# Kernel tuning notes

Hardware: AMD Instinct MI355X
Metric: run time of the kernel (lower is better)

The kernel has to match this reference:

```python
import jax, jax.numpy as jnp
import numpy as np

B, NA, NL, D = 512, 128, 512, 128
KA, KL = 16, 16  # active_agents, lane_tokens


def _layernorm(x, g, b, eps=1e-5):
    m = x.mean(-1, keepdims=True)
    v = ((x - m) ** 2).mean(-1, keepdims=True)
    return (x - m) / jnp.sqrt(v + eps) * g + b


def setup_inputs() -> dict:
    key = jax.random.key(0)
    ks = jax.random.split(key, 16)
    s = D ** -0.5
    inp = {
        "actor_feat": jax.random.normal(ks[0], (B, NA, D), jnp.float32),
        "lane_feat": jax.random.normal(ks[1], (B, NL, D), jnp.float32),
        "lane_centers": jax.random.normal(ks[2], (B, NL, 2), jnp.float32) * 50.0,
        "x_centers": jax.random.normal(ks[3], (B, NA, 2), jnp.float32) * 50.0,
        "spike_rate": jax.random.uniform(ks[4], (B, NA), jnp.float32),
        "actor_valid": jax.random.randint(ks[5], (B, NA), 0, 2).astype(bool),
        "lane_valid": jax.random.randint(ks[6], (B, NL), 0, 2).astype(bool),
        # MLP layer 0
        "W0a": jax.random.normal(ks[7], (D, D), jnp.float32) * s,
        "b0a": jnp.zeros((D,), jnp.float32),
        "W0b": jax.random.normal(ks[8], (D, D), jnp.float32) * s,
        "b0b": jnp.zeros((D,), jnp.float32),
        # MLP layer 1
        "W1a": jax.random.normal(ks[9], (D, D), jnp.float32) * s,
        "b1a": jnp.zeros((D,), jnp.float32),
        "W1b": jax.random.normal(ks[10], (D, D), jnp.float32) * s,
        "b1b": jnp.zeros((D,), jnp.float32),
        # shared LayerNorm
        "gamma": jnp.ones((D,), jnp.float32),
        "beta": jnp.zeros((D,), jnp.float32),
    }
    return inp


def reference(actor_feat, lane_feat, lane_centers, x_centers, spike_rate,
              actor_valid, lane_valid,
              W0a, b0a, W0b, b0b, W1a, b1a, W1b, b1b, gamma, beta):
    bsel = jnp.arange(B)[:, None]  # [B,1] batch index for fancy gather/scatter

    # masked top-k over spike_rate -> active agent indices [B,KA]
    masked = jnp.where(actor_valid, spike_rate, -jnp.inf)
    _, aidx = jax.lax.top_k(masked, KA)

    # lane selection: min distance from any active agent, k smallest
    ac = x_centers[bsel, aidx]                                # [B,KA,2]
    diff = ac[:, :, None, :] - lane_centers[:, None, :, :]    # [B,KA,NL,2]
    pair_dist = jnp.sqrt((diff ** 2).sum(-1))                 # cdist [B,KA,NL]
    lane_dist = pair_dist.min(axis=1)                         # [B,NL]
    lane_dist = jnp.where(lane_valid, lane_dist, jnp.inf)
    _, lidx = jax.lax.top_k(-lane_dist, KL)                   # k smallest

    # gather nodes and run residual MLP + LayerNorm stack
    nodes = jnp.concatenate([actor_feat[bsel, aidx], lane_feat[bsel, lidx]], axis=1)  # [B,KA+KL,D]
    for (Wa, ba, Wb, bb) in ((W0a, b0a, W0b, b0b), (W1a, b1a, W1b, b1b)):
        h = jax.nn.gelu(nodes @ Wa + ba, approximate=False) @ Wb + bb
        nodes = _layernorm(nodes + h, gamma, beta)

    # scatter updated nodes back into the full pools
    actor_out = actor_feat.at[bsel, aidx].set(nodes[:, :KA])
    lane_out = lane_feat.at[bsel, lidx].set(nodes[:, KA:])
    return actor_out, lane_out
```

## Files before the change

kernel.cpp:

```cpp
#include <hip/hip_runtime.h>
#include <math.h>

#define Bsz 512
#define NA  128
#define NL  512
#define Dd  128
#define KA  16
#define KL  16

#define NMLP  256
#define NCOPY 1280
#define PAIRS (Bsz * 320)

#define AIDX_OFF  0
#define LIDX_OFF  8192
#define AMASK_OFF 16384
#define LMASK_OFF 18432
#define FLAG_OFF  26624

typedef float nf4 __attribute__((ext_vector_type(4)));

__global__ __launch_bounds__(256) void detect_bool_kernel(
    const unsigned char* __restrict__ av, int* __restrict__ flag) {
  __shared__ int s;
  if (threadIdx.x == 0) s = 0;
  __syncthreads();
  int any = 0;
  for (int i = threadIdx.x; i < 4096; i += 256)
    if ((i & 3) && av[i]) any = 1;
  if (any) atomicOr(&s, 1);
  __syncthreads();
  if (threadIdx.x == 0) *flag = s;
}

__device__ __forceinline__ int validAt(const unsigned char* p, int i, int isbyte) {
  return isbyte ? (int)p[i] : ((const int*)p)[i];
}

__global__ __launch_bounds__(256) void idx_kernel(
    const float* __restrict__ spike, const unsigned char* __restrict__ avalid,
    const float* __restrict__ xc, const float* __restrict__ lc,
    const unsigned char* __restrict__ lvalid, const int* __restrict__ flagp,
    int* __restrict__ aidx, int* __restrict__ lidx,
    unsigned* __restrict__ amask_g, unsigned* __restrict__ lmask_g) {
  const int b = blockIdx.x;
  const int tid = threadIdx.x;
  const int isbyte = *flagp;

  __shared__ float s_ax[KA], s_ay[KA];
  __shared__ int   s_ai[KA];
  __shared__ int   s_li[KL];
  __shared__ float s_ld[NL];
  __shared__ float s_rv[4];
  __shared__ int   s_ri[4];
  __shared__ unsigned s_am[4], s_lm[16];

  if (tid < 64) {
    float v0 = validAt(avalid, b * NA + tid, isbyte)      ? spike[b * NA + tid]      : -INFINITY;
    float v1 = validAt(avalid, b * NA + tid + 64, isbyte) ? spike[b * NA + tid + 64] : -INFINITY;
    for (int it = 0; it < KA; ++it) {
      float bv = v0; int bi = tid;
      if (v1 > bv) { bv = v1; bi = tid + 64; }
      for (int off = 32; off; off >>= 1) {
        float ov = __shfl_xor(bv, off);
        int   oi = __shfl_xor(bi, off);
        if (ov > bv || (ov == bv && oi < bi)) { bv = ov; bi = oi; }
      }
      if (bi == tid)      v0 = -INFINITY;
      if (bi == tid + 64) v1 = -INFINITY;
      if (tid == 0) s_ai[it] = bi;
    }
  }
  __syncthreads();
  if (tid < KA) {
    int a = s_ai[tid];
    aidx[b * KA + tid] = a;
    s_ax[tid] = xc[(b * NA + a) * 2 + 0];
    s_ay[tid] = xc[(b * NA + a) * 2 + 1];
  }
  __syncthreads();

  for (int l = tid; l < NL; l += 256) {
    float lx = lc[(b * NL + l) * 2 + 0];
    float ly = lc[(b * NL + l) * 2 + 1];
    float best = INFINITY;
#pragma unroll
    for (int a = 0; a < KA; ++a) {
      float dx = s_ax[a] - lx, dy = s_ay[a] - ly;
      float d2 = __fadd_rn(__fmul_rn(dx, dx), __fmul_rn(dy, dy));
      best = fminf(best, d2);
    }
    best = sqrtf(best);
    s_ld[l] = validAt(lvalid, b * NL + l, isbyte) ? best : INFINITY;
  }
  __syncthreads();

  const int wid = tid >> 6, lane = tid & 63;
  for (int it = 0; it < KL; ++it) {
    float bv = s_ld[tid]; int bi = tid;
    float v2 = s_ld[tid + 256];
    if (v2 < bv) { bv = v2; bi = tid + 256; }
    for (int off = 32; off; off >>= 1) {
      float ov = __shfl_xor(bv, off);
      int   oi = __shfl_xor(bi, off);
      if (ov < bv || (ov == bv && oi < bi)) { bv = ov; bi = oi; }
    }
    if (lane == 0) { s_rv[wid] = bv; s_ri[wid] = bi; }
    __syncthreads();
    if (tid == 0) {
      float fbv = s_rv[0]; int fbi = s_ri[0];
      for (int w = 1; w < 4; ++w)
        if (s_rv[w] < fbv || (s_rv[w] == fbv && s_ri[w] < fbi)) { fbv = s_rv[w]; fbi = s_ri[w]; }
      lidx[b * KL + it] = fbi;
      s_li[it] = fbi;
      s_ld[fbi] = INFINITY;
    }
    __syncthreads();
  }

  if (tid < 4)  s_am[tid] = 0u;
  if (tid < 16) s_lm[tid] = 0u;
  __syncthreads();
  if (tid < 16) {
    int a = s_ai[tid];
    atomicOr(&s_am[a >> 5], 1u << (a & 31));
  } else if (tid < 32) {
    int l = s_li[tid - 16];
    atomicOr(&s_lm[l >> 5], 1u << (l & 31));
  }
  __syncthreads();
  if (tid < 4)  amask_g[b * 4 + tid]  = s_am[tid];
  if (tid < 16) lmask_g[b * 16 + tid] = s_lm[tid];
}


#define STAGE_LOAD(W, h)                                              \
  { const float4* wg4 = (const float4*)((W) + (h) * 8192);            \
    R0 = wg4[tid]; R1 = wg4[512 + tid];                               \
    R2 = wg4[1024 + tid]; R3 = wg4[1536 + tid]; }

#define STAGE_WRITE()                                                 \
  { float4* swg4 = (float4*)s_w;                                      \
    swg4[tid] = R0; swg4[512 + tid] = R1;                             \
    swg4[1024 + tid] = R2; swg4[1536 + tid] = R3; }

#define FMA_HALF(h)                                                   \
  _Pragma("unroll 4")                                                 \
  for (int g = 0; g < 16; ++g) {                                      \
    const float* wr = s_w + g * 4 * Dd;                               \
    float w00 = wr[j0],        w10 = wr[j1];                          \
    float w01 = wr[Dd + j0],   w11 = wr[Dd + j1];                     \
    float w02 = wr[2*Dd + j0], w12 = wr[2*Dd + j1];                   \
    float w03 = wr[3*Dd + j0], w13 = wr[3*Dd + j1];                   \
    _Pragma("unroll")                                                 \
    for (int n = 0; n < 8; ++n) {                                     \
      float4 xv = ((const float4*)s_xu[n0 + n])[(h) * 16 + g];        \
      acc0[n] = fmaf(xv.x, w00, acc0[n]); acc1[n] = fmaf(xv.x, w10, acc1[n]); \
      acc0[n] = fmaf(xv.y, w01, acc0[n]); acc1[n] = fmaf(xv.y, w11, acc1[n]); \
      acc0[n] = fmaf(xv.z, w02, acc0[n]); acc1[n] = fmaf(xv.z, w12, acc1[n]); \
      acc0[n] = fmaf(xv.w, w03, acc0[n]); acc1[n] = fmaf(xv.w, w13, acc1[n]); \
    }                                                                 \
  }

#define MATVEC(W, Bv)                                                 \
  { const float bias0 = (Bv)[j0], bias1 = (Bv)[j1];                   \
    _Pragma("unroll")                                                 \
    for (int n = 0; n < 8; ++n) { acc0[n] = bias0; acc1[n] = bias1; } \
    STAGE_LOAD(W, 0);                                                 \
    STAGE_WRITE(); __syncthreads();                                   \
    STAGE_LOAD(W, 1);                                                 \
    FMA_HALF(0);                                                      \
    __syncthreads();                                                  \
    STAGE_WRITE(); __syncthreads();                                   \
    FMA_HALF(1);                                                      \
    __syncthreads(); }

__global__ __launch_bounds__(512, 4) void fused_kernel(
    const float* __restrict__ actor_feat, const float* __restrict__ lane_feat,
    const int* __restrict__ aidx, const int* __restrict__ lidx,
    const unsigned* __restrict__ amask_g, const unsigned* __restrict__ lmask_g,
    const float* __restrict__ W0a, const float* __restrict__ b0a,
    const float* __restrict__ W0b, const float* __restrict__ b0b,
    const float* __restrict__ W1a, const float* __restrict__ b1a,
    const float* __restrict__ W1b, const float* __restrict__ b1b,
    const float* __restrict__ gamma, const float* __restrict__ beta,
    float* __restrict__ out0, float* __restrict__ out1) {
  __shared__ float s_w[64 * Dd];
  __shared__ float s_xu[64][Dd];
  __shared__ int   s_src[64];

  const int tid = threadIdx.x;
  const int wave = tid >> 6, lane = tid & 63;

  if (blockIdx.x < NMLP) {
    const int b0 = blockIdx.x * 2;
    if (tid < 64) {
      int rr = tid, bidx = b0 + (rr >> 5), lr = rr & 31;
      s_src[rr] = (lr < 16) ? aidx[bidx * KA + lr] : lidx[bidx * KL + lr - 16];
    }
    __syncthreads();

    const int n0 = wave * 8;
#pragma unroll
    for (int i = 0; i < 4; ++i) {
      int q = lane + 64 * i;
      int rr = n0 + (q >> 5), c4 = q & 31;
      int bidx = b0 + (rr >> 5), lr = rr & 31;
      const float* src = (lr < 16)
          ? actor_feat + ((size_t)bidx * NA + s_src[rr]) * Dd
          : lane_feat  + ((size_t)bidx * NL + s_src[rr]) * Dd;
      ((float4*)s_xu[rr])[c4] = ((const float4*)src)[c4];
    }

    const int j0 = lane, j1 = lane + 64;
    const float g0 = gamma[j0], g1 = gamma[j1];
    const float bt0 = beta[j0], bt1 = beta[j1];

    float acc0[8], acc1[8], rx0[8], rx1[8];
    float4 R0, R1, R2, R3;

#pragma unroll
    for (int n = 0; n < 8; ++n) {
      rx0[n] = s_xu[n0 + n][j0];
      rx1[n] = s_xu[n0 + n][j1];
    }

#pragma unroll 1
    for (int layer = 0; layer < 2; ++layer) {
      const float* wa = layer ? W1a : W0a;
      const float* ba = layer ? b1a : b0a;
      const float* wb = layer ? W1b : W0b;
      const float* bb = layer ? b1b : b0b;

      MATVEC(wa, ba);

#pragma unroll
      for (int n = 0; n < 8; ++n) {
        float t0 = acc0[n], t1 = acc1[n];
        s_xu[n0 + n][j0] = 0.5f * t0 * (1.0f + erff(t0 * 0.70710678118654752f));
        s_xu[n0 + n][j1] = 0.5f * t1 * (1.0f + erff(t1 * 0.70710678118654752f));
      }

      MATVEC(wb, bb);

#pragma unroll
      for (int n = 0; n < 8; ++n) {
        float r0 = rx0[n] + acc0[n];
        float r1 = rx1[n] + acc1[n];
        float sum = r0 + r1;
        for (int off = 32; off; off >>= 1) sum += __shfl_xor(sum, off);
        float mean = sum * (1.0f / 128.0f);
        float d0 = r0 - mean, d1 = r1 - mean;
        float sq = d0 * d0 + d1 * d1;
        for (int off = 32; off; off >>= 1) sq += __shfl_xor(sq, off);
        float inv = 1.0f / sqrtf(sq * (1.0f / 128.0f) + 1e-5f);
        float v0 = d0 * inv * g0 + bt0;
        float v1 = d1 * inv * g1 + bt1;
        if (layer == 0) {
          s_xu[n0 + n][j0] = v0; s_xu[n0 + n][j1] = v1;
          rx0[n] = v0; rx1[n] = v1;
        } else {
          int rr = n0 + n, bidx = b0 + (rr >> 5), lr = rr & 31, si = s_src[rr];
          float* dst = (lr < 16) ? out0 + ((size_t)bidx * NA + si) * Dd
                                 : out1 + ((size_t)bidx * NL + si) * Dd;
          dst[j0] = v0;
          dst[j1] = v1;
        }
      }
    }
  } else {
    const int gw = (blockIdx.x - NMLP) * 8 + wave;
    const int half = lane >> 5, c4 = lane & 31;
#pragma unroll 1
    for (int base = gw * 4; base < PAIRS; base += NCOPY * 8 * 4) {
      nf4 v[4]; int sel[4];
      const nf4* sp[4]; nf4* dp[4];
#pragma unroll
      for (int u = 0; u < 4; ++u) {
        int p = base + u;
        sel[u] = 1; sp[u] = 0; dp[u] = 0;
        if (p < PAIRS) {
          int b = p / 320;
          int pr = p - b * 320;
          int r = 2 * pr + half;
          unsigned mword; size_t prow;
          const float* srcpool; float* dstpool; int rbit;
          if (r < NA) {
            rbit = r;
            mword = amask_g[b * 4 + (r >> 5)];
            prow = (size_t)b * NA + r;
            srcpool = actor_feat; dstpool = out0;
          } else {
            int rl = r - NA;
            rbit = rl;
            mword = lmask_g[b * 16 + (rl >> 5)];
            prow = (size_t)b * NL + rl;
            srcpool = lane_feat; dstpool = out1;
          }
          sel[u] = (mword >> (rbit & 31)) & 1;
          sp[u] = (const nf4*)(srcpool + prow * Dd) + c4;
          dp[u] = (nf4*)(dstpool + prow * Dd) + c4;
          if (!sel[u]) v[u] = __builtin_nontemporal_load(sp[u]);
        }
      }
#pragma unroll
      for (int u = 0; u < 4; ++u)
        if (!sel[u]) __builtin_nontemporal_store(v[u], dp[u]);
    }
  }
}

extern "C" void kernel_launch(void* const* d_in, const int* in_sizes, int n_in,
                              void* d_out, int out_size, void* d_ws, size_t ws_size,
                              hipStream_t stream) {
  const float* actor_feat = (const float*)d_in[0];
  const float* lane_feat  = (const float*)d_in[1];
  const float* lc         = (const float*)d_in[2];
  const float* xc         = (const float*)d_in[3];
  const float* spike      = (const float*)d_in[4];
  const unsigned char* avalid = (const unsigned char*)d_in[5];
  const unsigned char* lvalid = (const unsigned char*)d_in[6];
  const float* W0a = (const float*)d_in[7];
  const float* b0a = (const float*)d_in[8];
  const float* W0b = (const float*)d_in[9];
  const float* b0b = (const float*)d_in[10];
  const float* W1a = (const float*)d_in[11];
  const float* b1a = (const float*)d_in[12];
  const float* W1b = (const float*)d_in[13];
  const float* b1b = (const float*)d_in[14];
  const float* gamma = (const float*)d_in[15];
  const float* beta  = (const float*)d_in[16];

  int* wsI = (int*)d_ws;
  int* aidx = wsI + AIDX_OFF;
  int* lidx = wsI + LIDX_OFF;
  unsigned* amask_g = (unsigned*)(wsI + AMASK_OFF);
  unsigned* lmask_g = (unsigned*)(wsI + LMASK_OFF);
  int* flag = wsI + FLAG_OFF;

  float* out0 = (float*)d_out;
  float* out1 = out0 + (size_t)Bsz * NA * Dd;

  detect_bool_kernel<<<1, 256, 0, stream>>>(avalid, flag);
  idx_kernel<<<Bsz, 256, 0, stream>>>(spike, avalid, xc, lc, lvalid, flag,
                                      aidx, lidx, amask_g, lmask_g);
  fused_kernel<<<NMLP + NCOPY, 512, 0, stream>>>(
      actor_feat, lane_feat, aidx, lidx, amask_g, lmask_g,
      W0a, b0a, W0b, b0b, W1a, b1a, W1b, b1b, gamma, beta, out0, out1);
}
```

Measured before the change: 122.3 us.

## Overlap full-pool copy with index selection and drop mask-based selective copy

```diff
diff --git a/kernel.cpp b/kernel.cpp
--- a/kernel.cpp
+++ b/kernel.cpp
@@ -8,56 +8,72 @@
 #define KA  16
 #define KL  16
 
-#define NMLP  256
-#define NCOPY 1280
-#define PAIRS (Bsz * 320)
-
-#define AIDX_OFF  0
-#define LIDX_OFF  8192
-#define AMASK_OFF 16384
-#define LMASK_OFF 18432
-#define FLAG_OFF  26624
-
-typedef float nf4 __attribute__((ext_vector_type(4)));
-
-__global__ __launch_bounds__(256) void detect_bool_kernel(
-    const unsigned char* __restrict__ av, int* __restrict__ flag) {
-  __shared__ int s;
-  if (threadIdx.x == 0) s = 0;
-  __syncthreads();
-  int any = 0;
-  for (int i = threadIdx.x; i < 4096; i += 256)
-    if ((i & 3) && av[i]) any = 1;
-  if (any) atomicOr(&s, 1);
-  __syncthreads();
-  if (threadIdx.x == 0) *flag = s;
-}
-
-__device__ __forceinline__ int validAt(const unsigned char* p, int i, int isbyte) {
-  return isbyte ? (int)p[i] : ((const int*)p)[i];
-}
-
-__global__ __launch_bounds__(256) void idx_kernel(
+#define NIDX  512
+#define NCB   3584
+#define ACT4  2097152
+#define TOT4  10485760
+#define CSTRIDE (NCB * 256)
+
+__global__ __launch_bounds__(256) void idx_copy_kernel(
     const float* __restrict__ spike, const unsigned char* __restrict__ avalid,
     const float* __restrict__ xc, const float* __restrict__ lc,
-    const unsigned char* __restrict__ lvalid, const int* __restrict__ flagp,
+    const unsigned char* __restrict__ lvalid,
+    const float* __restrict__ actor_feat, const float* __restrict__ lane_feat,
     int* __restrict__ aidx, int* __restrict__ lidx,
-    unsigned* __restrict__ amask_g, unsigned* __restrict__ lmask_g) {
+    float* __restrict__ out0, float* __restrict__ out1) {
+  const int tid = threadIdx.x;
+
+  if (blockIdx.x >= NIDX) {
+    const float4* __restrict__ srcA = (const float4*)actor_feat;
+    const float4* __restrict__ srcL = (const float4*)lane_feat;
+    float4* __restrict__ dstA = (float4*)out0;
+    float4* __restrict__ dstL = (float4*)out1;
+    const int gid = (blockIdx.x - NIDX) * 256 + tid;
+#pragma unroll 1
+    for (int base = gid; base < TOT4; base += 4 * CSTRIDE) {
+      float4 v[4]; int pp[4];
+#pragma unroll
+      for (int u = 0; u < 4; ++u) {
+        pp[u] = base + u * CSTRIDE;
+        if (pp[u] < TOT4)
+          v[u] = (pp[u] < ACT4) ? srcA[pp[u]] : srcL[pp[u] - ACT4];
+      }
+#pragma unroll
+      for (int u = 0; u < 4; ++u) {
+        if (pp[u] < TOT4) {
+          if (pp[u] < ACT4) dstA[pp[u]] = v[u];
+          else              dstL[pp[u] - ACT4] = v[u];
+        }
+      }
+    }
+    return;
+  }
+
   const int b = blockIdx.x;
-  const int tid = threadIdx.x;
-  const int isbyte = *flagp;
 
   __shared__ float s_ax[KA], s_ay[KA];
   __shared__ int   s_ai[KA];
-  __shared__ int   s_li[KL];
   __shared__ float s_ld[NL];
   __shared__ float s_rv[4];
   __shared__ int   s_ri[4];
-  __shared__ unsigned s_am[4], s_lm[16];
+  __shared__ int   s_flag;
+
+  if (tid == 0) s_flag = 0;
+  __syncthreads();
+  {
+    int any = 0;
+    for (int i = tid; i < 4096; i += 256)
+      if ((i & 3) && avalid[i]) any = 1;
+    if (any) atomicOr(&s_flag, 1);
+  }
+  __syncthreads();
+  const int isbyte = s_flag;
+
+#define VALID_AT(P, I) (isbyte ? (int)(P)[I] : ((const int*)(P))[I])
 
   if (tid < 64) {
-    float v0 = validAt(avalid, b * NA + tid, isbyte)      ? spike[b * NA + tid]      : -INFINITY;
-    float v1 = validAt(avalid, b * NA + tid + 64, isbyte) ? spike[b * NA + tid + 64] : -INFINITY;
+    float v0 = VALID_AT(avalid, b * NA + tid)      ? spike[b * NA + tid]      : -INFINITY;
+    float v1 = VALID_AT(avalid, b * NA + tid + 64) ? spike[b * NA + tid + 64] : -INFINITY;
     for (int it = 0; it < KA; ++it) {
       float bv = v0; int bi = tid;
       if (v1 > bv) { bv = v1; bi = tid + 64; }
@@ -91,7 +107,7 @@
       best = fminf(best, d2);
     }
     best = sqrtf(best);
-    s_ld[l] = validAt(lvalid, b * NL + l, isbyte) ? best : INFINITY;
+    s_ld[l] = VALID_AT(lvalid, b * NL + l) ? best : INFINITY;
   }
   __syncthreads();
 
@@ -112,25 +128,11 @@
       for (int w = 1; w < 4; ++w)
         if (s_rv[w] < fbv || (s_rv[w] == fbv && s_ri[w] < fbi)) { fbv = s_rv[w]; fbi = s_ri[w]; }
       lidx[b * KL + it] = fbi;
-      s_li[it] = fbi;
       s_ld[fbi] = INFINITY;
     }
     __syncthreads();
   }
-
-  if (tid < 4)  s_am[tid] = 0u;
-  if (tid < 16) s_lm[tid] = 0u;
-  __syncthreads();
-  if (tid < 16) {
-    int a = s_ai[tid];
-    atomicOr(&s_am[a >> 5], 1u << (a & 31));
-  } else if (tid < 32) {
-    int l = s_li[tid - 16];
-    atomicOr(&s_lm[l >> 5], 1u << (l & 31));
-  }
-  __syncthreads();
-  if (tid < 4)  amask_g[b * 4 + tid]  = s_am[tid];
-  if (tid < 16) lmask_g[b * 16 + tid] = s_lm[tid];
+#undef VALID_AT
 }
 
 
@@ -175,10 +177,9 @@
     FMA_HALF(1);                                                      \
     __syncthreads(); }
 
-__global__ __launch_bounds__(512, 4) void fused_kernel(
+__global__ __launch_bounds__(512, 2) void mlp_kernel(
     const float* __restrict__ actor_feat, const float* __restrict__ lane_feat,
     const int* __restrict__ aidx, const int* __restrict__ lidx,
-    const unsigned* __restrict__ amask_g, const unsigned* __restrict__ lmask_g,
     const float* __restrict__ W0a, const float* __restrict__ b0a,
     const float* __restrict__ W0b, const float* __restrict__ b0b,
     const float* __restrict__ W1a, const float* __restrict__ b1a,
@@ -191,121 +192,80 @@
 
   const int tid = threadIdx.x;
   const int wave = tid >> 6, lane = tid & 63;
-
-  if (blockIdx.x < NMLP) {
-    const int b0 = blockIdx.x * 2;
-    if (tid < 64) {
-      int rr = tid, bidx = b0 + (rr >> 5), lr = rr & 31;
-      s_src[rr] = (lr < 16) ? aidx[bidx * KA + lr] : lidx[bidx * KL + lr - 16];
-    }
-    __syncthreads();
-
-    const int n0 = wave * 8;
-#pragma unroll
-    for (int i = 0; i < 4; ++i) {
-      int q = lane + 64 * i;
-      int rr = n0 + (q >> 5), c4 = q & 31;
-      int bidx = b0 + (rr >> 5), lr = rr & 31;
-      const float* src = (lr < 16)
-          ? actor_feat + ((size_t)bidx * NA + s_src[rr]) * Dd
-          : lane_feat  + ((size_t)bidx * NL + s_src[rr]) * Dd;
-      ((float4*)s_xu[rr])[c4] = ((const float4*)src)[c4];
-    }
-
-    const int j0 = lane, j1 = lane + 64;
-    const float g0 = gamma[j0], g1 = gamma[j1];
-    const float bt0 = beta[j0], bt1 = beta[j1];
-
-    float acc0[8], acc1[8], rx0[8], rx1[8];
-    float4 R0, R1, R2, R3;
+  const int b0 = blockIdx.x * 2;
+
+  if (tid < 64) {
+    int rr = tid, bidx = b0 + (rr >> 5), lr = rr & 31;
+    s_src[rr] = (lr < 16) ? aidx[bidx * KA + lr] : lidx[bidx * KL + lr - 16];
+  }
+  __syncthreads();
+
+  const int n0 = wave * 8;
+#pragma unroll
+  for (int i = 0; i < 4; ++i) {
+    int q = lane + 64 * i;
+    int rr = n0 + (q >> 5), c4 = q & 31;
+    int bidx = b0 + (rr >> 5), lr = rr & 31;
+    const float* src = (lr < 16)
+        ? actor_feat + ((size_t)bidx * NA + s_src[rr]) * Dd
+        : lane_feat  + ((size_t)bidx * NL + s_src[rr]) * Dd;
+    ((float4*)s_xu[rr])[c4] = ((const float4*)src)[c4];
+  }
+
+  const int j0 = lane, j1 = lane + 64;
+  const float g0 = gamma[j0], g1 = gamma[j1];
+  const float bt0 = beta[j0], bt1 = beta[j1];
+
+  float acc0[8], acc1[8], rx0[8], rx1[8];
+  float4 R0, R1, R2, R3;
+
+#pragma unroll
+  for (int n = 0; n < 8; ++n) {
+    rx0[n] = s_xu[n0 + n][j0];
+    rx1[n] = s_xu[n0 + n][j1];
+  }
+
+#pragma unroll 1
+  for (int layer = 0; layer < 2; ++layer) {
+    const float* wa = layer ? W1a : W0a;
+    const float* ba = layer ? b1a : b0a;
+    const float* wb = layer ? W1b : W0b;
+    const float* bb = layer ? b1b : b0b;
+
+    MATVEC(wa, ba);
 
 #pragma unroll
     for (int n = 0; n < 8; ++n) {
-      rx0[n] = s_xu[n0 + n][j0];
-      rx1[n] = s_xu[n0 + n][j1];
-    }
-
-#pragma unroll 1
-    for (int layer = 0; layer < 2; ++layer) {
-      const float* wa = layer ? W1a : W0a;
-      const float* ba = layer ? b1a : b0a;
-      const float* wb = layer ? W1b : W0b;
-      const float* bb = layer ? b1b : b0b;
-
-      MATVEC(wa, ba);
-
-#pragma unroll
-      for (int n = 0; n < 8; ++n) {
-        float t0 = acc0[n], t1 = acc1[n];
-        s_xu[n0 + n][j0] = 0.5f * t0 * (1.0f + erff(t0 * 0.70710678118654752f));
-        s_xu[n0 + n][j1] = 0.5f * t1 * (1.0f + erff(t1 * 0.70710678118654752f));
+      float t0 = acc0[n], t1 = acc1[n];
+      s_xu[n0 + n][j0] = 0.5f * t0 * (1.0f + erff(t0 * 0.70710678118654752f));
+      s_xu[n0 + n][j1] = 0.5f * t1 * (1.0f + erff(t1 * 0.70710678118654752f));
+    }
+
+    MATVEC(wb, bb);
+
+#pragma unroll
+    for (int n = 0; n < 8; ++n) {
+      float r0 = rx0[n] + acc0[n];
+      float r1 = rx1[n] + acc1[n];
+      float sum = r0 + r1;
+      for (int off = 32; off; off >>= 1) sum += __shfl_xor(sum, off);
+      float mean = sum * (1.0f / 128.0f);
+      float d0 = r0 - mean, d1 = r1 - mean;
+      float sq = d0 * d0 + d1 * d1;
+      for (int off = 32; off; off >>= 1) sq += __shfl_xor(sq, off);
+      float inv = 1.0f / sqrtf(sq * (1.0f / 128.0f) + 1e-5f);
+      float v0 = d0 * inv * g0 + bt0;
+      float v1 = d1 * inv * g1 + bt1;
+      if (layer == 0) {
+        s_xu[n0 + n][j0] = v0; s_xu[n0 + n][j1] = v1;
+        rx0[n] = v0; rx1[n] = v1;
+      } else {
+        int rr = n0 + n, bidx = b0 + (rr >> 5), lr = rr & 31, si = s_src[rr];
+        float* dst = (lr < 16) ? out0 + ((size_t)bidx * NA + si) * Dd
+                               : out1 + ((size_t)bidx * NL + si) * Dd;
+        dst[j0] = v0;
+        dst[j1] = v1;
       }
-
-      MATVEC(wb, bb);
-
-#pragma unroll
-      for (int n = 0; n < 8; ++n) {
-        float r0 = rx0[n] + acc0[n];
-        float r1 = rx1[n] + acc1[n];
-        float sum = r0 + r1;
-        for (int off = 32; off; off >>= 1) sum += __shfl_xor(sum, off);
-        float mean = sum * (1.0f / 128.0f);
-        float d0 = r0 - mean, d1 = r1 - mean;
-        float sq = d0 * d0 + d1 * d1;
-        for (int off = 32; off; off >>= 1) sq += __shfl_xor(sq, off);
-        float inv = 1.0f / sqrtf(sq * (1.0f / 128.0f) + 1e-5f);
-        float v0 = d0 * inv * g0 + bt0;
-        float v1 = d1 * inv * g1 + bt1;
-        if (layer == 0) {
-          s_xu[n0 + n][j0] = v0; s_xu[n0 + n][j1] = v1;
-          rx0[n] = v0; rx1[n] = v1;
-        } else {
-          int rr = n0 + n, bidx = b0 + (rr >> 5), lr = rr & 31, si = s_src[rr];
-          float* dst = (lr < 16) ? out0 + ((size_t)bidx * NA + si) * Dd
-                                 : out1 + ((size_t)bidx * NL + si) * Dd;
-          dst[j0] = v0;
-          dst[j1] = v1;
-        }
-      }
-    }
-  } else {
-    const int gw = (blockIdx.x - NMLP) * 8 + wave;
-    const int half = lane >> 5, c4 = lane & 31;
-#pragma unroll 1
-    for (int base = gw * 4; base < PAIRS; base += NCOPY * 8 * 4) {
-      nf4 v[4]; int sel[4];
-      const nf4* sp[4]; nf4* dp[4];
-#pragma unroll
-      for (int u = 0; u < 4; ++u) {
-        int p = base + u;
-        sel[u] = 1; sp[u] = 0; dp[u] = 0;
-        if (p < PAIRS) {
-          int b = p / 320;
-          int pr = p - b * 320;
-          int r = 2 * pr + half;
-          unsigned mword; size_t prow;
-          const float* srcpool; float* dstpool; int rbit;
-          if (r < NA) {
-            rbit = r;
-            mword = amask_g[b * 4 + (r >> 5)];
-            prow = (size_t)b * NA + r;
-            srcpool = actor_feat; dstpool = out0;
-          } else {
-            int rl = r - NA;
-            rbit = rl;
-            mword = lmask_g[b * 16 + (rl >> 5)];
-            prow = (size_t)b * NL + rl;
-            srcpool = lane_feat; dstpool = out1;
-          }
-          sel[u] = (mword >> (rbit & 31)) & 1;
-          sp[u] = (const nf4*)(srcpool + prow * Dd) + c4;
-          dp[u] = (nf4*)(dstpool + prow * Dd) + c4;
-          if (!sel[u]) v[u] = __builtin_nontemporal_load(sp[u]);
-        }
-      }
-#pragma unroll
-      for (int u = 0; u < 4; ++u)
-        if (!sel[u]) __builtin_nontemporal_store(v[u], dp[u]);
     }
   }
 }
@@ -331,20 +291,16 @@
   const float* gamma = (const float*)d_in[15];
   const float* beta  = (const float*)d_in[16];
 
-  int* wsI = (int*)d_ws;
-  int* aidx = wsI + AIDX_OFF;
-  int* lidx = wsI + LIDX_OFF;
-  unsigned* amask_g = (unsigned*)(wsI + AMASK_OFF);
-  unsigned* lmask_g = (unsigned*)(wsI + LMASK_OFF);
-  int* flag = wsI + FLAG_OFF;
+  int* aidx = (int*)d_ws;
+  int* lidx = aidx + Bsz * KA;
 
   float* out0 = (float*)d_out;
   float* out1 = out0 + (size_t)Bsz * NA * Dd;
 
-  detect_bool_kernel<<<1, 256, 0, stream>>>(avalid, flag);
-  idx_kernel<<<Bsz, 256, 0, stream>>>(spike, avalid, xc, lc, lvalid, flag,
-                                      aidx, lidx, amask_g, lmask_g);
-  fused_kernel<<<NMLP + NCOPY, 512, 0, stream>>>(
-      actor_feat, lane_feat, aidx, lidx, amask_g, lmask_g,
+  idx_copy_kernel<<<NIDX + NCB, 256, 0, stream>>>(
+      spike, avalid, xc, lc, lvalid, actor_feat, lane_feat,
+      aidx, lidx, out0, out1);
+  mlp_kernel<<<Bsz / 2, 512, 0, stream>>>(
+      actor_feat, lane_feat, aidx, lidx,
       W0a, b0a, W0b, b0b, W1a, b1a, W1b, b1b, gamma, beta, out0, out1);
 }
```

New measurement: 141.0 us. +15.3%, slower.
